# Optimization experiments

Measured on AMD Instinct MI355X. Metric: run time of the kernel, lower is better.

## Reference

```python
import math
import jax, jax.numpy as jnp
import numpy as np
from jax.scipy.special import erf

BATCH, SEQ, DIM = 2, 4096, 128
EMA_HEADS, DQK, DV = 16, 64, 256
NUM_BUCKETS, MAX_DIST = 32, 128


def _next_fast_len(n):
    # smallest 5-smooth integer >= n (matches scipy.fftpack.next_fast_len)
    while True:
        m = n
        for p in (2, 3, 5):
            while m % p == 0:
                m //= p
        if m == 1:
            return n
        n += 1


def _laplacian_attn(x):
    mu = math.sqrt(0.5)
    std = math.sqrt(0.25 * math.pi)
    return 0.5 * (1.0 + erf((x - mu) / (std * math.sqrt(2.0))))


def _rel_pos_bias(table, n, scale):
    # causal T5 relative position bias, bucket(q_pos - k_pos)
    pos = jnp.arange(n)
    rel = jnp.maximum(pos[:, None] - pos[None, :], 0)  # [n, n], >= 0
    max_exact = NUM_BUCKETS // 2
    is_small = rel < max_exact
    val_large = max_exact + (
        jnp.log(jnp.maximum(rel, 1).astype(jnp.float32) / max_exact)
        / math.log(MAX_DIST / max_exact) * (NUM_BUCKETS - max_exact)
    ).astype(jnp.int32)
    val_large = jnp.minimum(val_large, NUM_BUCKETS - 1)
    bucket = jnp.where(is_small, rel, val_large)
    return table[bucket, 0] * scale  # [n, n]


def _conv1d_fft(x, K, n):
    # x: [b, n, h, d] (fft over axis 1), K: [n, h] (fft over axis 0)
    fast_len = _next_fast_len(2 * n - 1)
    f_x = jnp.fft.rfft(x, n=fast_len, axis=1)
    f_K = jnp.fft.rfft(K, n=fast_len, axis=0)
    out = jnp.fft.irfft(f_x * jnp.conj(f_K)[None, :, :, None], fast_len, axis=1)
    out = jnp.roll(out, -1, axis=1)
    return out[:, fast_len - n:]  # [b, n, h, d]


def _forward(x, expansion, reduction, alphas, dampen, Wqk, bqk, gamma, beta,
             Wv, bv, rel_table, Wr, br, Wu, bu, Wh, Uh, bh):
    b, n, d = x.shape
    # ---- multi-headed EMA (causal -> unidirectional) via FFT conv ----
    xe = jnp.einsum('bnd,hd->bnhd', x, expansion)
    a = jax.nn.sigmoid(alphas)            # [h]
    dm = jax.nn.sigmoid(dampen)           # [h]
    powers = jnp.arange(n - 1, -1, -1, dtype=x.dtype)  # reversed powers
    K = a * ((1.0 - a) * dm) ** powers[:, None]        # [n, h]
    conv = _conv1d_fft(xe, K, n)
    ema = jnp.einsum('bnhd,hd->bnd', conv, reduction)  # [b, n, d]
    # ---- single-headed attention (chunk_size=-1 -> one chunk), v from x ----
    qk = jax.nn.silu(ema @ Wqk + bqk)     # [b, n, dqk]
    q = qk * gamma[0] + beta[0]
    k = qk * gamma[1] + beta[1]
    v = jax.nn.silu(x @ Wv + bv)          # [b, n, dv]
    scale = 1.0 / n                       # laplacian_attn_fn scaling
    sim = jnp.einsum('bid,bjd->bij', q, k) * scale
    sim = sim + _rel_pos_bias(rel_table, n, DQK ** 0.5)
    attn = _laplacian_attn(sim)
    causal_mask = jnp.triu(jnp.ones((n, n), dtype=bool), 1)
    attn = jnp.where(causal_mask, 0.0, attn)  # laplacian: zero after activation
    attn_out = jnp.einsum('bij,bjd->bid', attn, v)  # [b, n, dv]
    # ---- gating + output ----
    reset_gate = jax.nn.silu(ema @ Wr + br)         # [b, n, dv]
    update_gate = jax.nn.sigmoid(ema @ Wu + bu)     # [b, n, d]
    gated = attn_out * reset_gate
    H = jax.nn.silu(ema @ Wh + gated @ Uh + bh)     # [b, n, d]
    return update_gate * H + (1.0 - update_gate) * x


def setup_inputs() -> dict:
    key = jax.random.key(0)
    ks = jax.random.split(key, 18)
    def rn(i, shape, s=1.0):
        return jax.random.normal(ks[i], shape, dtype=jnp.float32) * s
    return dict(
        x=rn(0, (BATCH, SEQ, DIM)),
        expansion=rn(1, (EMA_HEADS, DIM), 0.2),
        reduction=rn(2, (EMA_HEADS, DIM), 0.2),
        alphas=rn(3, (EMA_HEADS,)),
        dampen=rn(4, (EMA_HEADS,)),
        Wqk=rn(5, (DIM, DQK), 0.05), bqk=rn(6, (DQK,), 0.02),
        gamma=rn(7, (2, DQK), 0.02), beta=jnp.zeros((2, DQK), jnp.float32),
        Wv=rn(8, (DIM, DV), 0.05), bv=rn(9, (DV,), 0.02),
        rel_table=rn(10, (NUM_BUCKETS, 1), 0.02),
        Wr=rn(11, (DIM, DV), 0.05), br=rn(12, (DV,), 0.02),
        Wu=rn(13, (DIM, DIM), 0.05), bu=rn(14, (DIM,), 0.02),
        Wh=rn(15, (DIM, DIM), 0.05), Uh=rn(16, (DV, DIM), 0.05),
        bh=rn(17, (DIM,), 0.02),
    )


def reference(x, expansion, reduction, alphas, dampen, Wqk, bqk, gamma, beta,
              Wv, bv, rel_table, Wr, br, Wu, bu, Wh, Uh, bh):
    return _forward(x, expansion, reduction, alphas, dampen, Wqk, bqk, gamma,
                    beta, Wv, bv, rel_table, Wr, br, Wu, bu, Wh, Uh, bh)
```

## Files before the change

### kernel.cpp

```cpp
#include <hip/hip_runtime.h>
#include <cstdint>
#include <cmath>

#define B_ 2
#define N_ 4096
#define D_ 128
#define H_ 16
#define DQK_ 64
#define DV_ 256

typedef float    f4_t  __attribute__((ext_vector_type(4)));
typedef float    f16f  __attribute__((ext_vector_type(16)));
typedef _Float16 h4_t  __attribute__((ext_vector_type(4)));
typedef _Float16 h8_t  __attribute__((ext_vector_type(8)));

__device__ __forceinline__ float sigmoidf_(float z) { return 1.f/(1.f + expf(-z)); }
__device__ __forceinline__ float siluf_(float z)    { return z/(1.f + expf(-z)); }
__device__ __forceinline__ f16f zero16() {
  f16f z;
#pragma unroll
  for (int i = 0; i < 16; ++i) z[i] = 0.f;
  return z;
}

__global__ void ema_phase1(const float* __restrict__ x, const float* __restrict__ expansion,
                           const float* __restrict__ alphas, const float* __restrict__ dampen,
                           float* __restrict__ F, _Float16* __restrict__ xh) {
  int bid = blockIdx.x;
  int dg = bid & 7, c = (bid >> 3) & 63, b = bid >> 9;
  int h = threadIdx.x & 15, dl = threadIdx.x >> 4;
  int d = dg*16 + dl;
  float a  = sigmoidf_(alphas[h]);
  float dm = sigmoidf_(dampen[h]);
  float q  = (1.f - a)*dm;
  float coef = a * expansion[h*D_ + d];
  __shared__ float xs[64][16];
  {
    int e = threadIdx.x;
    int t = e >> 2, seg = e & 3;
    const float* xp = x + ((size_t)b*N_ + c*64 + t)*D_ + dg*16 + seg*4;
    f4_t v = *(const f4_t*)xp;
    *(f4_t*)&xs[t][seg*4] = v;
    h4_t hv;
#pragma unroll
    for (int j = 0; j < 4; ++j) hv[j] = (_Float16)v[j];
    *(h4_t*)(xh + ((size_t)b*N_ + c*64 + t)*D_ + dg*16 + seg*4) = hv;
  }
  __syncthreads();
  float s = 0.f;
#pragma unroll
  for (int t = 0; t < 64; ++t) s = fmaf(q, s, coef*xs[t][dl]);
  F[(((size_t)b*H_ + h)*D_ + d)*64 + c] = s;
}

__global__ void ema_carry(const float* __restrict__ F, const float* __restrict__ alphas,
                          const float* __restrict__ dampen, float* __restrict__ carry) {
  int idx = blockIdx.x*256 + threadIdx.x;
  int h = (idx >> 7) & 15;
  float a  = sigmoidf_(alphas[h]);
  float dm = sigmoidf_(dampen[h]);
  float q  = (1.f - a)*dm;
  float qL = q;
#pragma unroll
  for (int i = 0; i < 6; ++i) qL *= qL;
  const float* Fp = F + (size_t)idx*64;
  float* cp = carry + (size_t)idx*64;
  float s = 0.f;
  for (int cc = 0; cc < 64; ++cc) { cp[cc] = s; s = fmaf(qL, s, Fp[cc]); }
}

__global__ void ema_phase2(const float* __restrict__ x, const float* __restrict__ expansion,
                           const float* __restrict__ reduction,
                           const float* __restrict__ alphas, const float* __restrict__ dampen,
                           const float* __restrict__ carry, _Float16* __restrict__ emah) {
  int bid = blockIdx.x;
  int dg = bid & 7, c = (bid >> 3) & 63, b = bid >> 9;
  int h = threadIdx.x & 15, dl = threadIdx.x >> 4;
  int d = dg*16 + dl;
  float a  = sigmoidf_(alphas[h]);
  float dm = sigmoidf_(dampen[h]);
  float q  = (1.f - a)*dm;
  float coef = a * expansion[h*D_ + d];
  float red  = reduction[h*D_ + d];
  __shared__ float xs[64][16];
  {
    int e = threadIdx.x;
    int t = e >> 2, seg = e & 3;
    const float* xp = x + ((size_t)b*N_ + c*64 + t)*D_ + dg*16 + seg*4;
    *(f4_t*)&xs[t][seg*4] = *(const f4_t*)xp;
  }
  __syncthreads();
  float s = carry[(((size_t)b*H_ + h)*D_ + d)*64 + c];
  for (int t = 0; t < 64; ++t) {
    s = fmaf(q, s, coef*xs[t][dl]);
    float v = red * s;
    v += __shfl_xor(v, 1); v += __shfl_xor(v, 2);
    v += __shfl_xor(v, 4); v += __shfl_xor(v, 8);
    if (h == 0) emah[((size_t)b*N_ + c*64 + t)*D_ + d] = (_Float16)v;
  }
}

__global__ void prep_all(const float* __restrict__ Wqk, const float* __restrict__ Wv,
                         const float* __restrict__ Wr, const float* __restrict__ Wu,
                         const float* __restrict__ Wh,
                         const float* __restrict__ bqk, const float* __restrict__ bv,
                         const float* __restrict__ br, const float* __restrict__ bu,
                         const float* __restrict__ bh,
                         const float* __restrict__ Uh, const float* __restrict__ rel_table,
                         _Float16* __restrict__ Wt, float* __restrict__ bcat,
                         _Float16* __restrict__ Uht, float* __restrict__ bias2T) {
  int idx = blockIdx.x*256 + threadIdx.x;
  if (idx < 832*128) {
    int c = idx >> 7, d = idx & 127;
    const float* W; const float* bias; int ncol, cl;
    if (c < 64)       { W=Wqk; bias=bqk; ncol=64;  cl=c; }
    else if (c < 320) { W=Wv;  bias=bv;  ncol=256; cl=c-64; }
    else if (c < 576) { W=Wr;  bias=br;  ncol=256; cl=c-320; }
    else if (c < 704) { W=Wu;  bias=bu;  ncol=128; cl=c-576; }
    else              { W=Wh;  bias=bh;  ncol=128; cl=c-704; }
    Wt[idx] = (_Float16)W[d*ncol + cl];
    if (d == 0) bcat[c] = bias[cl];
  } else if (idx < 832*128 + 32768) {
    int i2 = idx - 832*128;
    int k = i2 >> 7, c = i2 & 127;
    Uht[(size_t)c*256 + k] = (_Float16)Uh[i2];
  } else if (idx < 832*128 + 32768 + 4096) {
    int r = idx - (832*128 + 32768);
    int bucket;
    if (r < 16) bucket = r;
    else {
      double v = log((double)r / 16.0) / log(8.0) * 16.0;
      bucket = 16 + (int)v;
      if (bucket > 31) bucket = 31;
    }
    bias2T[r] = (rel_table[bucket]*8.0f - 0.70710678f) * 1.1283792f;
  }
}

__global__ __launch_bounds__(256) void linear_mfma(
    const _Float16* __restrict__ emah, const _Float16* __restrict__ xh,
    const _Float16* __restrict__ Wt, const float* __restrict__ bcat,
    const float* __restrict__ gamma, const float* __restrict__ beta,
    _Float16* __restrict__ qh, _Float16* __restrict__ kh, _Float16* __restrict__ vTt,
    float* __restrict__ resetb, float* __restrict__ updateb, float* __restrict__ hemab) {
  int slab = blockIdx.x % 13, rt = blockIdx.x / 13;
  int tid = threadIdx.x;
  int lane = tid & 63, w = tid >> 6;
  int lr = lane & 15, lg = lane >> 4;
  int mode = (slab==0)?0:(slab<5)?1:(slab<9)?2:(slab<11)?3:4;
  const _Float16* src = (mode==1) ? xh : emah;
  __shared__ _Float16 As[64][136];
  __shared__ _Float16 Ws[64][136];
  {
    const h8_t* s8 = (const h8_t*)(src + (size_t)rt*64*D_);
#pragma unroll
    for (int i = 0; i < 4; ++i) {
      int idx = tid + i*256;
      int row = idx >> 4, seg = idx & 15;
      *(h8_t*)&As[row][seg*8] = s8[idx];
    }
    const h8_t* w8 = (const h8_t*)(Wt + (size_t)slab*64*D_);
#pragma unroll
    for (int i = 0; i < 4; ++i) {
      int idx = tid + i*256;
      int row = idx >> 4, seg = idx & 15;
      *(h8_t*)&Ws[row][seg*8] = w8[idx];
    }
  }
  __syncthreads();
  h4_t af[8];
#pragma unroll
  for (int ks = 0; ks < 8; ++ks) af[ks] = *(const h4_t*)&As[w*16 + lr][ks*16 + lg*4];
  int row0 = rt*64 + w*16 + lg*4;
#pragma unroll
  for (int ns = 0; ns < 4; ++ns) {
    f4_t acc = (f4_t){0.f,0.f,0.f,0.f};
#pragma unroll
    for (int ks = 0; ks < 8; ++ks) {
      h4_t bf = *(const h4_t*)&Ws[ns*16 + lr][ks*16 + lg*4];
      acc = __builtin_amdgcn_mfma_f32_16x16x16f16(af[ks], bf, acc, 0, 0, 0);
    }
    int c = slab*64 + ns*16 + lr;
    float bias = bcat[c];
    if (mode == 0) {
      float g0 = gamma[c], g1 = gamma[64+c], be0 = beta[c], be1 = beta[64+c];
#pragma unroll
      for (int r = 0; r < 4; ++r) {
        float qk = siluf_(acc[r] + bias);
        size_t row = row0 + r;
        qh[row*DQK_ + c] = (_Float16)(qk*g0 + be0);
        kh[row*DQK_ + c] = (_Float16)(qk*g1 + be1);
      }
    } else if (mode == 1) {
      int cl = c - 64;
      int bb = row0 >> 12, rl = row0 & 4095;
      h4_t vv;
#pragma unroll
      for (int r = 0; r < 4; ++r) vv[r] = (_Float16)siluf_(acc[r] + bias);
      *(h4_t*)&vTt[(((size_t)bb*128 + (rl>>5))*256 + cl)*32 + (rl&31)] = vv;
    } else if (mode == 2) {
      int cl = c - 320;
#pragma unroll
      for (int r = 0; r < 4; ++r) resetb[(size_t)(row0 + r)*DV_ + cl] = siluf_(acc[r] + bias);
    } else if (mode == 3) {
      int cl = c - 576;
#pragma unroll
      for (int r = 0; r < 4; ++r) updateb[(size_t)(row0 + r)*D_ + cl] = sigmoidf_(acc[r] + bias);
    } else {
      int cl = c - 704;
#pragma unroll
      for (int r = 0; r < 4; ++r) hemab[(size_t)(row0 + r)*D_ + cl] = acc[r] + bias;
    }
  }
}

__global__ __launch_bounds__(256, 3) void attn_kernel(
    const _Float16* __restrict__ qh, const _Float16* __restrict__ kh,
    const _Float16* __restrict__ vTt, const float* __restrict__ bias2T,
    _Float16* __restrict__ attnp) {
  int bid = blockIdx.x;
  int it = 63 - (bid >> 5);
  int rem = bid & 31;
  int s = rem >> 1, b = rem & 1;
  int a = it >> 2, r = it & 3;
  int nblk = a + 1;
  if (s >= nblk) return;
  int T = 2*it + 2;
  int tlo = (s*T)/nblk, thi = ((s+1)*T)/nblk;
  int nt = thi - tlo;
  int base = it + 2*a*(a-1) + r*a;
  int slot = base + s;
  int i0 = it * 64;
  int tid = threadIdx.x;
  int lane = tid & 63, w = tid >> 6;
  int ih = w & 1;
  int dvh = w >> 1;
  bool prod = (dvh == 0);
  int lm = lane & 31, lg = lane >> 5;

  __shared__ __align__(16) char Vb[2][18432];
  __shared__ __align__(16) char Kb[2][4352];
  __shared__ __align__(16) char Pb[2][2560];
  __shared__ float biasW[320];

  int jmaxv = thi*32 - 1;
  int dlo = i0 - jmaxv;
  int cnt = 64 + jmaxv - tlo*32;
  for (int k = tid; k < cnt; k += 256) {
    int d = dlo + k;
    biasW[k] = d < 0 ? -1e38f : bias2T[d];
  }

  h4_t qf[8];
  if (prod) {
    const _Float16* qp = qh + ((size_t)b*N_ + i0 + ih*32 + lm)*DQK_ + 4*lg;
#pragma unroll
    for (int ksq = 0; ksq < 8; ++ksq) qf[ksq] = *(const h4_t*)(qp + 8*ksq);
  }

  f16f accO[4];
#pragma unroll
  for (int i = 0; i < 4; ++i) accO[i] = zero16();

  const _Float16* kbase = kh + (size_t)b*N_*DQK_;
  const _Float16* vbase = vTt + (size_t)b*128*8192;
  int st = tid & 127;
  int kr = st >> 2, ks16 = st & 3;

  h8_t k8a, k8b, vr[8];
#define ISSUE_(JT) { \
  const _Float16* kp_ = kbase + (size_t)((JT)*32 + kr)*DQK_ + ks16*16; \
  k8a = *(const h8_t*)kp_; k8b = *(const h8_t*)(kp_ + 8); \
  const _Float16* vp_ = vbase + (size_t)(JT)*8192 + st*32; \
  _Pragma("unroll") for (int i = 0; i < 4; ++i) vr[i] = *(const h8_t*)(vp_ + i*8); \
  _Pragma("unroll") for (int i = 0; i < 4; ++i) vr[4+i] = *(const h8_t*)(vp_ + 4096 + i*8); }

#define COMMIT_(BI) { \
  char* kb_ = Kb[BI] + kr*136 + ks16*32; \
  *(h4_t*)kb_        = __builtin_shufflevector(k8a, k8a, 0,1,2,3); \
  *(h4_t*)(kb_ + 8)  = __builtin_shufflevector(k8a, k8a, 4,5,6,7); \
  *(h4_t*)(kb_ + 16) = __builtin_shufflevector(k8b, k8b, 0,1,2,3); \
  *(h4_t*)(kb_ + 24) = __builtin_shufflevector(k8b, k8b, 4,5,6,7); \
  char* va_ = Vb[BI] + st*72; \
  _Pragma("unroll") for (int i = 0; i < 4; ++i) { \
    *(h4_t*)(va_ + i*16)     = __builtin_shufflevector(vr[i], vr[i], 0,1,2,3); \
    *(h4_t*)(va_ + i*16 + 8) = __builtin_shufflevector(vr[i], vr[i], 4,5,6,7); } \
  char* vb2_ = Vb[BI] + (st + 128)*72; \
  _Pragma("unroll") for (int i = 0; i < 4; ++i) { \
    *(h4_t*)(vb2_ + i*16)     = __builtin_shufflevector(vr[4+i], vr[4+i], 0,1,2,3); \
    *(h4_t*)(vb2_ + i*16 + 8) = __builtin_shufflevector(vr[4+i], vr[4+i], 4,5,6,7); } }

  if (!prod) {
    ISSUE_(tlo);
    COMMIT_(0);
    if (nt > 1) ISSUE_(tlo + 1);
  }
  __syncthreads();

  const float C1 = 1.1283792f / 4096.f;
  int ibase = i0 + ih*32 + lm;
#pragma unroll 1
  for (int t = 0; t < nt; ++t) {
    h4_t pa[4];
    if (prod) {
      const char* kb = Kb[t & 1];
      __builtin_amdgcn_s_setprio(1);
      f16f accS = zero16();
#pragma unroll
      for (int ksq = 0; ksq < 8; ++ksq) {
        h4_t kf = *(const h4_t*)(kb + lm*136 + 16*ksq + 8*lg);
        accS = __builtin_amdgcn_mfma_f32_32x32x8f16(kf, qf[ksq], accS, 0, 0, 0);
      }
      __builtin_amdgcn_s_setprio(0);
      int idx0 = ibase - dlo - (tlo + t)*32 - 4*lg;
#pragma unroll
      for (int rr = 0; rr < 16; ++rr) {
        float tt = fmaf(accS[rr], C1, biasW[idx0 - 8*(rr>>2) - (rr&3)]);
        float e = tt*fmaf(tt*tt, -0.101797f, -2.304877f);
        float u = exp2f(e);
        float pv = __builtin_amdgcn_rcpf(1.f + u);
        pa[rr>>2][rr&3] = (_Float16)pv;
      }
      char* pp = Pb[ih] + lane*40;
#pragma unroll
      for (int k2 = 0; k2 < 4; ++k2) *(h4_t*)(pp + k2*8) = pa[k2];
    } else {
      if (t+1 < nt) COMMIT_((t+1) & 1);
      if (t+2 < nt) ISSUE_(tlo + t + 2);
    }
    __syncthreads();
    if (!prod) {
      const char* pp = Pb[ih] + lane*40;
#pragma unroll
      for (int k2 = 0; k2 < 4; ++k2) pa[k2] = *(const h4_t*)(pp + k2*8);
    }
    const char* vb = Vb[t & 1];
    __builtin_amdgcn_s_setprio(1);
#pragma unroll
    for (int ks = 0; ks < 4; ++ks) {
#pragma unroll
      for (int dvb = 0; dvb < 4; ++dvb) {
        h4_t vf = *(const h4_t*)(vb + (dvh*128 + dvb*32 + lm)*72 + 16*ks + 8*lg);
        accO[dvb] = __builtin_amdgcn_mfma_f32_32x32x8f16(pa[ks], vf, accO[dvb], 0, 0, 0);
      }
    }
    __builtin_amdgcn_s_setprio(0);
    __syncthreads();
  }
#undef ISSUE_
#undef COMMIT_

  _Float16* op = attnp + ((size_t)b*544 + slot)*(64*256);
#pragma unroll
  for (int dvb = 0; dvb < 4; ++dvb) {
    int col = dvh*128 + dvb*32 + lm;
#pragma unroll
    for (int rr = 0; rr < 16; ++rr) {
      int row = ih*32 + 8*(rr>>2) + 4*lg + (rr&3);
      op[(size_t)row*256 + col] = (_Float16)accO[dvb][rr];
    }
  }
}

__global__ void combine_gated(const _Float16* __restrict__ attnp, const float* __restrict__ resetb,
                              _Float16* __restrict__ gatedh) {
  size_t fi = (size_t)blockIdx.x*256 + threadIdx.x;
  int c4 = (int)(fi & 63);
  int rr = (int)(fi >> 6);
  int b = rr >> 12, n = rr & 4095;
  int it = n >> 6, rowLocal = n & 63;
  int a = it >> 2, r = it & 3;
  int nblk = a + 1;
  int base = it + 2*a*(a-1) + r*a;
  const _Float16* ap = attnp + ((size_t)b*544 + base)*16384 + rowLocal*256 + c4*4;
  f4_t acc = (f4_t){0.f,0.f,0.f,0.f};
  for (int s2 = 0; s2 < nblk; ++s2) {
    h4_t pv = *(const h4_t*)(ap + (size_t)s2*16384);
#pragma unroll
    for (int j = 0; j < 4; ++j) acc[j] += (float)pv[j];
  }
  f4_t rg = ((const f4_t*)resetb)[fi];
  f4_t g = acc * rg;
  h4_t hg;
#pragma unroll
  for (int j = 0; j < 4; ++j) hg[j] = (_Float16)g[j];
  *(h4_t*)(gatedh + fi*4) = hg;
}

__global__ __launch_bounds__(256) void final_mfma(
    const _Float16* __restrict__ gatedh, const _Float16* __restrict__ Uht,
    const float* __restrict__ hemab, const float* __restrict__ updateb,
    const float* __restrict__ x, float* __restrict__ out) {
  int rt = blockIdx.x >> 1, cs = blockIdx.x & 1;
  int tid = threadIdx.x;
  int lane = tid & 63, w = tid >> 6;
  int lr = lane & 15, lg = lane >> 4;
  int row0 = rt*64, c0 = cs*64;
  __shared__ _Float16 As[64][136];
  __shared__ _Float16 Ws[64][136];
  f4_t acc[4];
#pragma unroll
  for (int ns = 0; ns < 4; ++ns) acc[ns] = (f4_t){0.f,0.f,0.f,0.f};
#pragma unroll
  for (int kc = 0; kc < 2; ++kc) {
    __syncthreads();
#pragma unroll
    for (int i = 0; i < 4; ++i) {
      int idx = tid + i*256;
      int row = idx >> 4, seg = idx & 15;
      *(h8_t*)&As[row][seg*8] =
          *(const h8_t*)(gatedh + (size_t)(row0 + row)*DV_ + kc*128 + seg*8);
      *(h8_t*)&Ws[row][seg*8] =
          *(const h8_t*)(Uht + (size_t)(c0 + row)*DV_ + kc*128 + seg*8);
    }
    __syncthreads();
    h4_t af[8];
#pragma unroll
    for (int ks = 0; ks < 8; ++ks) af[ks] = *(const h4_t*)&As[w*16 + lr][ks*16 + lg*4];
#pragma unroll
    for (int ns = 0; ns < 4; ++ns) {
#pragma unroll
      for (int ks = 0; ks < 8; ++ks) {
        h4_t bf = *(const h4_t*)&Ws[ns*16 + lr][ks*16 + lg*4];
        acc[ns] = __builtin_amdgcn_mfma_f32_16x16x16f16(af[ks], bf, acc[ns], 0, 0, 0);
      }
    }
  }
  int orow = row0 + w*16 + lg*4;
#pragma unroll
  for (int ns = 0; ns < 4; ++ns) {
    int col = c0 + ns*16 + lr;
#pragma unroll
    for (int r = 0; r < 4; ++r) {
      size_t o = (size_t)(orow + r)*D_ + col;
      float z = acc[ns][r] + hemab[o];
      float Hv = siluf_(z);
      float u  = updateb[o];
      out[o] = u*Hv + (1.f - u)*x[o];
    }
  }
}

extern "C" void kernel_launch(void* const* d_in, const int* in_sizes, int n_in,
                              void* d_out, int out_size, void* d_ws, size_t ws_size,
                              hipStream_t stream) {
  (void)in_sizes; (void)n_in; (void)out_size; (void)ws_size;
  const float* x         = (const float*)d_in[0];
  const float* expansion = (const float*)d_in[1];
  const float* reduction = (const float*)d_in[2];
  const float* alphas    = (const float*)d_in[3];
  const float* dampen    = (const float*)d_in[4];
  const float* Wqk       = (const float*)d_in[5];
  const float* bqk       = (const float*)d_in[6];
  const float* gamma     = (const float*)d_in[7];
  const float* beta      = (const float*)d_in[8];
  const float* Wv        = (const float*)d_in[9];
  const float* bv        = (const float*)d_in[10];
  const float* rel_table = (const float*)d_in[11];
  const float* Wr        = (const float*)d_in[12];
  const float* br        = (const float*)d_in[13];
  const float* Wu        = (const float*)d_in[14];
  const float* bu        = (const float*)d_in[15];
  const float* Wh        = (const float*)d_in[16];
  const float* Uh        = (const float*)d_in[17];
  const float* bh        = (const float*)d_in[18];
  float* out = (float*)d_out;

  char* p = (char*)d_ws;
  size_t off = 0;
  auto alloc = [&](size_t bytes) -> char* {
    char* r = p + off;
    off += (bytes + 255) & ~(size_t)255;
    return r;
  };
  float*    F      = (float*)alloc((size_t)B_*H_*D_*64*4);
  float*    carry  = (float*)alloc((size_t)B_*H_*D_*64*4);
  _Float16* emah   = (_Float16*)alloc((size_t)B_*N_*D_*2);
  _Float16* xh     = (_Float16*)alloc((size_t)B_*N_*D_*2);
  float*    bias2T = (float*)alloc((size_t)N_*4);
  _Float16* Wt     = (_Float16*)alloc((size_t)832*128*2);
  float*    bcat   = (float*)alloc((size_t)832*4);
  _Float16* Uht    = (_Float16*)alloc((size_t)D_*DV_*2);
  _Float16* qh     = (_Float16*)alloc((size_t)B_*N_*DQK_*2);
  _Float16* kh     = (_Float16*)alloc((size_t)B_*N_*DQK_*2);
  _Float16* vTt    = (_Float16*)alloc((size_t)B_*DV_*N_*2);
  float*    resetb = (float*)alloc((size_t)B_*N_*DV_*4);
  float*    updateb= (float*)alloc((size_t)B_*N_*D_*4);
  float*    hemab  = (float*)alloc((size_t)B_*N_*D_*4);
  _Float16* gatedh = (_Float16*)alloc((size_t)B_*N_*DV_*2);
  _Float16* attnp  = (_Float16*)alloc((size_t)B_*544*64*256*2);

  prep_all<<<560, 256, 0, stream>>>(Wqk, Wv, Wr, Wu, Wh, bqk, bv, br, bu, bh,
                                    Uh, rel_table, Wt, bcat, Uht, bias2T);
  ema_phase1<<<1024, 256, 0, stream>>>(x, expansion, alphas, dampen, F, xh);
  ema_carry<<<16, 256, 0, stream>>>(F, alphas, dampen, carry);
  ema_phase2<<<1024, 256, 0, stream>>>(x, expansion, reduction, alphas, dampen, carry, emah);
  linear_mfma<<<128*13, 256, 0, stream>>>(emah, xh, Wt, bcat, gamma, beta,
                                          qh, kh, vTt, resetb, updateb, hemab);
  attn_kernel<<<2048, 256, 0, stream>>>(qh, kh, vTt, bias2T, attnp);
  combine_gated<<<2048, 256, 0, stream>>>(attnp, resetb, gatedh);
  final_mfma<<<256, 256, 0, stream>>>(gatedh, Uht, hemab, updateb, x, out);
}
```

Before: 113.8 us.

## Parallel-scan EMA carry, fp16 gate buffers, 128-row attention tiles

```diff
diff --git a/kernel.cpp b/kernel.cpp
--- a/kernel.cpp
+++ b/kernel.cpp
@@ -55,18 +55,25 @@
 
 __global__ void ema_carry(const float* __restrict__ F, const float* __restrict__ alphas,
                           const float* __restrict__ dampen, float* __restrict__ carry) {
-  int idx = blockIdx.x*256 + threadIdx.x;
-  int h = (idx >> 7) & 15;
+  int wid = blockIdx.x*4 + (threadIdx.x >> 6);
+  int lane = threadIdx.x & 63;
+  int h = (wid >> 7) & 15;
   float a  = sigmoidf_(alphas[h]);
   float dm = sigmoidf_(dampen[h]);
   float q  = (1.f - a)*dm;
   float qL = q;
 #pragma unroll
   for (int i = 0; i < 6; ++i) qL *= qL;
-  const float* Fp = F + (size_t)idx*64;
-  float* cp = carry + (size_t)idx*64;
-  float s = 0.f;
-  for (int cc = 0; cc < 64; ++cc) { cp[cc] = s; s = fmaf(qL, s, Fp[cc]); }
+  float A = qL;
+  float Bv = F[(size_t)wid*64 + lane];
+#pragma unroll
+  for (int len = 1; len < 64; len <<= 1) {
+    float Ap = __shfl_up(A, len);
+    float Bp = __shfl_up(Bv, len);
+    if (lane >= len) { Bv = fmaf(A, Bp, Bv); A = A*Ap; }
+  }
+  float Bprev = __shfl_up(Bv, 1);
+  carry[(size_t)wid*64 + lane] = (lane == 0) ? 0.f : Bprev;
 }
 
 __global__ void ema_phase2(const float* __restrict__ x, const float* __restrict__ expansion,
@@ -142,7 +149,8 @@
     const _Float16* __restrict__ Wt, const float* __restrict__ bcat,
     const float* __restrict__ gamma, const float* __restrict__ beta,
     _Float16* __restrict__ qh, _Float16* __restrict__ kh, _Float16* __restrict__ vTt,
-    float* __restrict__ resetb, float* __restrict__ updateb, float* __restrict__ hemab) {
+    _Float16* __restrict__ resetbh, _Float16* __restrict__ updatebh,
+    float* __restrict__ hemab) {
   int slab = blockIdx.x % 13, rt = blockIdx.x / 13;
   int tid = threadIdx.x;
   int lane = tid & 63, w = tid >> 6;
@@ -201,11 +209,13 @@
     } else if (mode == 2) {
       int cl = c - 320;
 #pragma unroll
-      for (int r = 0; r < 4; ++r) resetb[(size_t)(row0 + r)*DV_ + cl] = siluf_(acc[r] + bias);
+      for (int r = 0; r < 4; ++r)
+        resetbh[(size_t)(row0 + r)*DV_ + cl] = (_Float16)siluf_(acc[r] + bias);
     } else if (mode == 3) {
       int cl = c - 576;
 #pragma unroll
-      for (int r = 0; r < 4; ++r) updateb[(size_t)(row0 + r)*D_ + cl] = sigmoidf_(acc[r] + bias);
+      for (int r = 0; r < 4; ++r)
+        updatebh[(size_t)(row0 + r)*D_ + cl] = (_Float16)sigmoidf_(acc[r] + bias);
     } else {
       int cl = c - 704;
 #pragma unroll
@@ -214,46 +224,46 @@
   }
 }
 
-__global__ __launch_bounds__(256, 3) void attn_kernel(
+__global__ __launch_bounds__(512, 2) void attn_kernel(
     const _Float16* __restrict__ qh, const _Float16* __restrict__ kh,
     const _Float16* __restrict__ vTt, const float* __restrict__ bias2T,
     _Float16* __restrict__ attnp) {
   int bid = blockIdx.x;
-  int it = 63 - (bid >> 5);
+  int ip = 31 - (bid >> 5);
   int rem = bid & 31;
   int s = rem >> 1, b = rem & 1;
-  int a = it >> 2, r = it & 3;
-  int nblk = a + 1;
+  int nblk = (ip + 2) >> 1;
   if (s >= nblk) return;
-  int T = 2*it + 2;
+  int T = 4*ip + 4;
   int tlo = (s*T)/nblk, thi = ((s+1)*T)/nblk;
   int nt = thi - tlo;
-  int base = it + 2*a*(a-1) + r*a;
+  int tq = ip >> 1;
+  int base = (ip & 1) ? (tq+1)*(tq+1) : tq*(tq+1);
   int slot = base + s;
-  int i0 = it * 64;
+  int i0 = ip*128;
   int tid = threadIdx.x;
   int lane = tid & 63, w = tid >> 6;
-  int ih = w & 1;
-  int dvh = w >> 1;
+  int iq = w & 3;
+  int dvh = w >> 2;
   bool prod = (dvh == 0);
   int lm = lane & 31, lg = lane >> 5;
 
   __shared__ __align__(16) char Vb[2][18432];
   __shared__ __align__(16) char Kb[2][4352];
-  __shared__ __align__(16) char Pb[2][2560];
-  __shared__ float biasW[320];
+  __shared__ __align__(16) char Pb[2][4][2560];
+  __shared__ float biasW[384];
 
   int jmaxv = thi*32 - 1;
   int dlo = i0 - jmaxv;
-  int cnt = 64 + jmaxv - tlo*32;
-  for (int k = tid; k < cnt; k += 256) {
+  int cnt = 128 + jmaxv - tlo*32;
+  for (int k = tid; k < cnt; k += 512) {
     int d = dlo + k;
     biasW[k] = d < 0 ? -1e38f : bias2T[d];
   }
 
   h4_t qf[8];
   if (prod) {
-    const _Float16* qp = qh + ((size_t)b*N_ + i0 + ih*32 + lm)*DQK_ + 4*lg;
+    const _Float16* qp = qh + ((size_t)b*N_ + i0 + iq*32 + lm)*DQK_ + 4*lg;
 #pragma unroll
     for (int ksq = 0; ksq < 8; ++ksq) qf[ksq] = *(const h4_t*)(qp + 8*ksq);
   }
@@ -264,31 +274,23 @@
 
   const _Float16* kbase = kh + (size_t)b*N_*DQK_;
   const _Float16* vbase = vTt + (size_t)b*128*8192;
-  int st = tid & 127;
-  int kr = st >> 2, ks16 = st & 3;
-
-  h8_t k8a, k8b, vr[8];
+  int st = tid & 255;
+  int kr = st >> 3, kc = st & 7;
+
+  h8_t k8r, vr4[4];
 #define ISSUE_(JT) { \
-  const _Float16* kp_ = kbase + (size_t)((JT)*32 + kr)*DQK_ + ks16*16; \
-  k8a = *(const h8_t*)kp_; k8b = *(const h8_t*)(kp_ + 8); \
+  k8r = *(const h8_t*)(kbase + (size_t)((JT)*32 + kr)*DQK_ + kc*8); \
   const _Float16* vp_ = vbase + (size_t)(JT)*8192 + st*32; \
-  _Pragma("unroll") for (int i = 0; i < 4; ++i) vr[i] = *(const h8_t*)(vp_ + i*8); \
-  _Pragma("unroll") for (int i = 0; i < 4; ++i) vr[4+i] = *(const h8_t*)(vp_ + 4096 + i*8); }
+  _Pragma("unroll") for (int i = 0; i < 4; ++i) vr4[i] = *(const h8_t*)(vp_ + i*8); }
 
 #define COMMIT_(BI) { \
-  char* kb_ = Kb[BI] + kr*136 + ks16*32; \
-  *(h4_t*)kb_        = __builtin_shufflevector(k8a, k8a, 0,1,2,3); \
-  *(h4_t*)(kb_ + 8)  = __builtin_shufflevector(k8a, k8a, 4,5,6,7); \
-  *(h4_t*)(kb_ + 16) = __builtin_shufflevector(k8b, k8b, 0,1,2,3); \
-  *(h4_t*)(kb_ + 24) = __builtin_shufflevector(k8b, k8b, 4,5,6,7); \
+  char* ka_ = Kb[BI] + kr*136 + kc*16; \
+  *(h4_t*)ka_       = __builtin_shufflevector(k8r, k8r, 0,1,2,3); \
+  *(h4_t*)(ka_ + 8) = __builtin_shufflevector(k8r, k8r, 4,5,6,7); \
   char* va_ = Vb[BI] + st*72; \
   _Pragma("unroll") for (int i = 0; i < 4; ++i) { \
-    *(h4_t*)(va_ + i*16)     = __builtin_shufflevector(vr[i], vr[i], 0,1,2,3); \
-    *(h4_t*)(va_ + i*16 + 8) = __builtin_shufflevector(vr[i], vr[i], 4,5,6,7); } \
-  char* vb2_ = Vb[BI] + (st + 128)*72; \
-  _Pragma("unroll") for (int i = 0; i < 4; ++i) { \
-    *(h4_t*)(vb2_ + i*16)     = __builtin_shufflevector(vr[4+i], vr[4+i], 0,1,2,3); \
-    *(h4_t*)(vb2_ + i*16 + 8) = __builtin_shufflevector(vr[4+i], vr[4+i], 4,5,6,7); } }
+    *(h4_t*)(va_ + i*16)     = __builtin_shufflevector(vr4[i], vr4[i], 0,1,2,3); \
+    *(h4_t*)(va_ + i*16 + 8) = __builtin_shufflevector(vr4[i], vr4[i], 4,5,6,7); } }
 
   if (!prod) {
     ISSUE_(tlo);
@@ -298,7 +300,7 @@
   __syncthreads();
 
   const float C1 = 1.1283792f / 4096.f;
-  int ibase = i0 + ih*32 + lm;
+  int ibase = i0 + iq*32 + lm;
 #pragma unroll 1
   for (int t = 0; t < nt; ++t) {
     h4_t pa[4];
@@ -321,7 +323,7 @@
         float pv = __builtin_amdgcn_rcpf(1.f + u);
         pa[rr>>2][rr&3] = (_Float16)pv;
       }
-      char* pp = Pb[ih] + lane*40;
+      char* pp = Pb[t & 1][iq] + lane*40;
 #pragma unroll
       for (int k2 = 0; k2 < 4; ++k2) *(h4_t*)(pp + k2*8) = pa[k2];
     } else {
@@ -330,7 +332,7 @@
     }
     __syncthreads();
     if (!prod) {
-      const char* pp = Pb[ih] + lane*40;
+      const char* pp = Pb[t & 1][iq] + lane*40;
 #pragma unroll
       for (int k2 = 0; k2 < 4; ++k2) pa[k2] = *(const h4_t*)(pp + k2*8);
     }
@@ -350,46 +352,46 @@
 #undef ISSUE_
 #undef COMMIT_
 
-  _Float16* op = attnp + ((size_t)b*544 + slot)*(64*256);
+  _Float16* op = attnp + ((size_t)b*272 + slot)*(128*256);
 #pragma unroll
   for (int dvb = 0; dvb < 4; ++dvb) {
     int col = dvh*128 + dvb*32 + lm;
 #pragma unroll
     for (int rr = 0; rr < 16; ++rr) {
-      int row = ih*32 + 8*(rr>>2) + 4*lg + (rr&3);
+      int row = iq*32 + 8*(rr>>2) + 4*lg + (rr&3);
       op[(size_t)row*256 + col] = (_Float16)accO[dvb][rr];
     }
   }
 }
 
-__global__ void combine_gated(const _Float16* __restrict__ attnp, const float* __restrict__ resetb,
+__global__ void combine_gated(const _Float16* __restrict__ attnp,
+                              const _Float16* __restrict__ resetbh,
                               _Float16* __restrict__ gatedh) {
   size_t fi = (size_t)blockIdx.x*256 + threadIdx.x;
   int c4 = (int)(fi & 63);
   int rr = (int)(fi >> 6);
   int b = rr >> 12, n = rr & 4095;
-  int it = n >> 6, rowLocal = n & 63;
-  int a = it >> 2, r = it & 3;
-  int nblk = a + 1;
-  int base = it + 2*a*(a-1) + r*a;
-  const _Float16* ap = attnp + ((size_t)b*544 + base)*16384 + rowLocal*256 + c4*4;
+  int ip = n >> 7, rowLocal = n & 127;
+  int nblk = (ip + 2) >> 1;
+  int tq = ip >> 1;
+  int base = (ip & 1) ? (tq+1)*(tq+1) : tq*(tq+1);
+  const _Float16* ap = attnp + ((size_t)b*272 + base)*32768 + (size_t)rowLocal*256 + c4*4;
   f4_t acc = (f4_t){0.f,0.f,0.f,0.f};
   for (int s2 = 0; s2 < nblk; ++s2) {
-    h4_t pv = *(const h4_t*)(ap + (size_t)s2*16384);
+    h4_t pv = *(const h4_t*)(ap + (size_t)s2*32768);
 #pragma unroll
     for (int j = 0; j < 4; ++j) acc[j] += (float)pv[j];
   }
-  f4_t rg = ((const f4_t*)resetb)[fi];
-  f4_t g = acc * rg;
+  h4_t rg = *(const h4_t*)(resetbh + fi*4);
   h4_t hg;
 #pragma unroll
-  for (int j = 0; j < 4; ++j) hg[j] = (_Float16)g[j];
+  for (int j = 0; j < 4; ++j) hg[j] = (_Float16)(acc[j] * (float)rg[j]);
   *(h4_t*)(gatedh + fi*4) = hg;
 }
 
 __global__ __launch_bounds__(256) void final_mfma(
     const _Float16* __restrict__ gatedh, const _Float16* __restrict__ Uht,
-    const float* __restrict__ hemab, const float* __restrict__ updateb,
+    const float* __restrict__ hemab, const _Float16* __restrict__ updatebh,
     const float* __restrict__ x, float* __restrict__ out) {
   int rt = blockIdx.x >> 1, cs = blockIdx.x & 1;
   int tid = threadIdx.x;
@@ -435,7 +437,7 @@
       size_t o = (size_t)(orow + r)*D_ + col;
       float z = acc[ns][r] + hemab[o];
       float Hv = siluf_(z);
-      float u  = updateb[o];
+      float u  = (float)updatebh[o];
       out[o] = u*Hv + (1.f - u)*x[o];
     }
   }
@@ -473,31 +475,31 @@
     off += (bytes + 255) & ~(size_t)255;
     return r;
   };
-  float*    F      = (float*)alloc((size_t)B_*H_*D_*64*4);
-  float*    carry  = (float*)alloc((size_t)B_*H_*D_*64*4);
-  _Float16* emah   = (_Float16*)alloc((size_t)B_*N_*D_*2);
-  _Float16* xh     = (_Float16*)alloc((size_t)B_*N_*D_*2);
-  float*    bias2T = (float*)alloc((size_t)N_*4);
-  _Float16* Wt     = (_Float16*)alloc((size_t)832*128*2);
-  float*    bcat   = (float*)alloc((size_t)832*4);
-  _Float16* Uht    = (_Float16*)alloc((size_t)D_*DV_*2);
-  _Float16* qh     = (_Float16*)alloc((size_t)B_*N_*DQK_*2);
-  _Float16* kh     = (_Float16*)alloc((size_t)B_*N_*DQK_*2);
-  _Float16* vTt    = (_Float16*)alloc((size_t)B_*DV_*N_*2);
-  float*    resetb = (float*)alloc((size_t)B_*N_*DV_*4);
-  float*    updateb= (float*)alloc((size_t)B_*N_*D_*4);
-  float*    hemab  = (float*)alloc((size_t)B_*N_*D_*4);
-  _Float16* gatedh = (_Float16*)alloc((size_t)B_*N_*DV_*2);
-  _Float16* attnp  = (_Float16*)alloc((size_t)B_*544*64*256*2);
+  float*    F       = (float*)alloc((size_t)B_*H_*D_*64*4);
+  float*    carry   = (float*)alloc((size_t)B_*H_*D_*64*4);
+  _Float16* emah    = (_Float16*)alloc((size_t)B_*N_*D_*2);
+  _Float16* xh      = (_Float16*)alloc((size_t)B_*N_*D_*2);
+  float*    bias2T  = (float*)alloc((size_t)N_*4);
+  _Float16* Wt      = (_Float16*)alloc((size_t)832*128*2);
+  float*    bcat    = (float*)alloc((size_t)832*4);
+  _Float16* Uht     = (_Float16*)alloc((size_t)D_*DV_*2);
+  _Float16* qh      = (_Float16*)alloc((size_t)B_*N_*DQK_*2);
+  _Float16* kh      = (_Float16*)alloc((size_t)B_*N_*DQK_*2);
+  _Float16* vTt     = (_Float16*)alloc((size_t)B_*DV_*N_*2);
+  _Float16* resetbh = (_Float16*)alloc((size_t)B_*N_*DV_*2);
+  _Float16* updatebh= (_Float16*)alloc((size_t)B_*N_*D_*2);
+  float*    hemab   = (float*)alloc((size_t)B_*N_*D_*4);
+  _Float16* gatedh  = (_Float16*)alloc((size_t)B_*N_*DV_*2);
+  _Float16* attnp   = (_Float16*)alloc((size_t)B_*272*128*256*2);
 
   prep_all<<<560, 256, 0, stream>>>(Wqk, Wv, Wr, Wu, Wh, bqk, bv, br, bu, bh,
                                     Uh, rel_table, Wt, bcat, Uht, bias2T);
   ema_phase1<<<1024, 256, 0, stream>>>(x, expansion, alphas, dampen, F, xh);
-  ema_carry<<<16, 256, 0, stream>>>(F, alphas, dampen, carry);
+  ema_carry<<<1024, 256, 0, stream>>>(F, alphas, dampen, carry);
   ema_phase2<<<1024, 256, 0, stream>>>(x, expansion, reduction, alphas, dampen, carry, emah);
   linear_mfma<<<128*13, 256, 0, stream>>>(emah, xh, Wt, bcat, gamma, beta,
-                                          qh, kh, vTt, resetb, updateb, hemab);
-  attn_kernel<<<2048, 256, 0, stream>>>(qh, kh, vTt, bias2T, attnp);
-  combine_gated<<<2048, 256, 0, stream>>>(attnp, resetb, gatedh);
-  final_mfma<<<256, 256, 0, stream>>>(gatedh, Uht, hemab, updateb, x, out);
-}
+                                          qh, kh, vTt, resetbh, updatebh, hemab);
+  attn_kernel<<<1024, 512, 0, stream>>>(qh, kh, vTt, bias2T, attnp);
+  combine_gated<<<2048, 256, 0, stream>>>(attnp, resetbh, gatedh);
+  final_mfma<<<256, 256, 0, stream>>>(gatedh, Uht, hemab, updatebh, x, out);
+}
```

Result: slower. 122.5 us (+7.6%).
